# Optimization experiments

Hardware: AMD Instinct MI355X
Metric: run time of the kernel (lower is better)

The kernel has to match this reference:

```python
import jax, jax.numpy as jnp
import numpy as np

B, N, C = 16, 2048, 512
EPS = 1e-9        # numerical_stabilizer
BN_EPS = 1e-5     # flax BatchNorm default epsilon


def setup_inputs() -> dict:
    key = jax.random.key(0)
    ks = jax.random.split(key, 9)
    s = 1.0 / np.sqrt(C)

    def w(k):
        return jax.random.normal(k, (C, C), jnp.float32) * s

    return {
        "x": jax.random.normal(ks[0], (B, N, C), jnp.float32),
        "Wq": w(ks[1]), "bq": jnp.zeros((C,), jnp.float32),
        "Wk": w(ks[2]), "bk": jnp.zeros((C,), jnp.float32),
        "Wv": w(ks[3]), "bv": jnp.zeros((C,), jnp.float32),
        "Wo": w(ks[4]), "bo": jnp.zeros((C,), jnp.float32),
        "bn_scale": jnp.ones((C,), jnp.float32),
        "bn_bias": jnp.zeros((C,), jnp.float32),
        "bn_mean": jnp.zeros((C,), jnp.float32),
        "bn_var": jnp.ones((C,), jnp.float32),
    }


def reference(x, Wq, bq, Wk, bk, Wv, bv, Wo, bo,
              bn_scale, bn_bias, bn_mean, bn_var):
    # 1x1 'Conv' projections == pointwise linear layers
    q = x @ Wq + bq                                   # [B,N,C]
    k = x @ Wk + bk
    v = x @ Wv + bv

    # attention scores + row softmax
    att = jax.nn.softmax(jnp.einsum('bmc,bnc->bmn', q, k), axis=-1)  # [B,M,N]

    # post-softmax column renormalization: A / (eps + sum_M A),
    # then einsum '...MN,...NC->...NC' contracts M, so the effective
    # per-point scale is colsum / (eps + colsum).
    col = jnp.sum(att, axis=1)                        # [B,N]
    scale = col / (EPS + col)                         # [B,N]
    out = scale[..., None] * v                        # [B,N,C]

    # attention_type == 'naive': no offset
    y = out @ Wo + bo
    # BatchNorm with running stats (train=False)
    y = (y - bn_mean) * jax.lax.rsqrt(bn_var + BN_EPS) * bn_scale + bn_bias
    return jax.nn.relu(y) + x
```

## Files before the change

### kernel.cpp

```cpp
#include <hip/hip_runtime.h>
#include <math.h>

#define BB 16
#define NN 2048
#define CC 512
#define MM (BB * NN)
#define NSPLIT 4

typedef _Float16 half8 __attribute__((ext_vector_type(8)));
typedef _Float16 half4 __attribute__((ext_vector_type(4)));
typedef float floatx4 __attribute__((ext_vector_type(4)));

#define GLD16(gp, lp) __builtin_amdgcn_global_load_lds( \
    (const __attribute__((address_space(1))) void*)(gp), \
    (__attribute__((address_space(3))) void*)(lp), 16, 0, 0)

__device__ __forceinline__ int foff(int row16base, int fr, int g4) {
    return (row16base + fr) * 32 + ((g4 ^ ((fr >> 1) & 3)) << 3);
}

__global__ __launch_bounds__(256)
void calc_w2(const float* __restrict__ Wk, const float* __restrict__ bq,
             float* __restrict__ w2)
{
    const int i = blockIdx.x * 256 + threadIdx.x;
    if (i < 512) {
        float s = 0.0f;
        for (int j = 0; j < 512; ++j) s += Wk[i * 512 + j] * bq[j];
        w2[i] = s;
    }
}

__global__ __launch_bounds__(256)
void split_x_beta(const float* __restrict__ x, const float* __restrict__ w2,
                  _Float16* __restrict__ xh, _Float16* __restrict__ xl,
                  float* __restrict__ bet)
{
    __shared__ float part[4];
    const int t = threadIdx.x;
    const size_t i = (size_t)blockIdx.x * 1024 + (size_t)t * 4;
    const float4 v = *(const float4*)(x + i);
    half4 h, l;
    h[0] = (_Float16)v.x; l[0] = (_Float16)(v.x - (float)h[0]);
    h[1] = (_Float16)v.y; l[1] = (_Float16)(v.y - (float)h[1]);
    h[2] = (_Float16)v.z; l[2] = (_Float16)(v.z - (float)h[2]);
    h[3] = (_Float16)v.w; l[3] = (_Float16)(v.w - (float)h[3]);
    *(half4*)(xh + i) = h;
    *(half4*)(xl + i) = l;

    const float4 wv = *(const float4*)(w2 + ((t * 4) & 511));
    float s = v.x * wv.x + v.y * wv.y + v.z * wv.z + v.w * wv.w;
#pragma unroll
    for (int off = 1; off < 64; off <<= 1) s += __shfl_xor(s, off);
    const int w = t >> 6;
    if ((t & 63) == 0) part[w] = s;
    __syncthreads();
    const int m0 = blockIdx.x * 2;
    if (t == 0)   bet[m0]     = part[0] + part[1];
    if (t == 128) bet[m0 + 1] = part[2] + part[3];
}

__global__ __launch_bounds__(256)
void conv_wT(const float* __restrict__ W, _Float16* __restrict__ Wt)
{
    const int o = blockIdx.x * 256 + threadIdx.x;
    const int n = o >> 9, k = o & 511;
    Wt[o] = (_Float16)W[k * 512 + n];
}

__global__ __launch_bounds__(256)
void gemm_nt_split(const float* __restrict__ A, const float* __restrict__ Bm,
                   _Float16* __restrict__ outh, _Float16* __restrict__ outl)
{
    __shared__ float As[16][64];
    __shared__ float Bs[16][64];
    const int t = threadIdx.x, tc = t & 15, tr = t >> 4;
    const int j0 = blockIdx.x * 64, i0 = blockIdx.y * 64;
    const int lm = t >> 2, lk4 = (t & 3) << 2;
    float acc[4][4] = {};
    for (int kt = 0; kt < 512; kt += 16) {
        const float4 xa = *(const float4*)(A + (size_t)(j0 + lm) * 512 + kt + lk4);
        As[lk4 + 0][lm] = xa.x; As[lk4 + 1][lm] = xa.y;
        As[lk4 + 2][lm] = xa.z; As[lk4 + 3][lm] = xa.w;
        const float4 xb = *(const float4*)(Bm + (size_t)(i0 + lm) * 512 + kt + lk4);
        Bs[lk4 + 0][lm] = xb.x; Bs[lk4 + 1][lm] = xb.y;
        Bs[lk4 + 2][lm] = xb.z; Bs[lk4 + 3][lm] = xb.w;
        __syncthreads();
#pragma unroll
        for (int k = 0; k < 16; ++k) {
            float av[4], bv[4];
            *(float4*)av = *(const float4*)&As[k][tr * 4];
            *(float4*)bv = *(const float4*)&Bs[k][tc * 4];
#pragma unroll
            for (int i = 0; i < 4; ++i)
#pragma unroll
                for (int j = 0; j < 4; ++j)
                    acc[i][j] = fmaf(av[i], bv[j], acc[i][j]);
        }
        __syncthreads();
    }
#pragma unroll
    for (int i = 0; i < 4; ++i) {
        const int row = j0 + tr * 4 + i;
#pragma unroll
        for (int j = 0; j < 4; ++j) {
            const int col = i0 + tc * 4 + j;
            const float y = acc[i][j];
            const _Float16 h = (_Float16)y;
            outh[row * 512 + col] = h;
            outl[row * 512 + col] = (_Float16)(y - (float)h);
        }
    }
}

__global__ __launch_bounds__(256)
void gemm16_split(const _Float16* __restrict__ Ah, const _Float16* __restrict__ Al,
                  const _Float16* __restrict__ Bh, const _Float16* __restrict__ Bl,
                  _Float16* __restrict__ oh, _Float16* __restrict__ ol)
{
    __shared__ __align__(16) _Float16 sAh[128 * 32], sBh[128 * 32];
    __shared__ __align__(16) _Float16 sAl[128 * 32], sBl[128 * 32];

    const int t = threadIdx.x, lane = t & 63, w = t >> 6;
    const int m0 = blockIdx.x * 128, n0 = blockIdx.y * 128;
    const int lr4 = lane >> 2;
    const int sw8 = (((lane & 3) ^ ((lr4 >> 1) & 3)) << 3);
    const int fr = lane & 15, g4 = lane >> 4;
    const int wr = (w >> 1) * 64, wc = (w & 1) * 64;

    floatx4 acc[4][4];
#pragma unroll
    for (int i = 0; i < 4; ++i)
#pragma unroll
        for (int j = 0; j < 4; ++j) acc[i][j] = (floatx4){0.f, 0.f, 0.f, 0.f};

    for (int kt = 0; kt < CC; kt += 32) {
#pragma unroll
        for (int c = 0; c < 2; ++c) {
            const int r = w * 32 + c * 16;
            const size_t goA = (size_t)(m0 + r + lr4) * CC + kt + sw8;
            const size_t goB = (size_t)(n0 + r + lr4) * CC + kt + sw8;
            GLD16(Ah + goA, sAh + r * 32);
            GLD16(Bh + goB, sBh + r * 32);
            GLD16(Al + goA, sAl + r * 32);
            GLD16(Bl + goB, sBl + r * 32);
        }
        __syncthreads();

        half8 fa[4], fb[4], fal[4], fbl[4];
#pragma unroll
        for (int rt = 0; rt < 4; ++rt) {
            fa[rt]  = *(const half8*)&sAh[foff(wr + rt * 16, fr, g4)];
            fal[rt] = *(const half8*)&sAl[foff(wr + rt * 16, fr, g4)];
        }
#pragma unroll
        for (int ct = 0; ct < 4; ++ct) {
            fb[ct]  = *(const half8*)&sBh[foff(wc + ct * 16, fr, g4)];
            fbl[ct] = *(const half8*)&sBl[foff(wc + ct * 16, fr, g4)];
        }
#pragma unroll
        for (int rt = 0; rt < 4; ++rt)
#pragma unroll
            for (int ct = 0; ct < 4; ++ct) {
                acc[rt][ct] = __builtin_amdgcn_mfma_f32_16x16x32_f16(
                    fa[rt], fb[ct], acc[rt][ct], 0, 0, 0);
                acc[rt][ct] = __builtin_amdgcn_mfma_f32_16x16x32_f16(
                    fa[rt], fbl[ct], acc[rt][ct], 0, 0, 0);
                acc[rt][ct] = __builtin_amdgcn_mfma_f32_16x16x32_f16(
                    fal[rt], fb[ct], acc[rt][ct], 0, 0, 0);
            }
        __syncthreads();
    }

#pragma unroll
    for (int rt = 0; rt < 4; ++rt)
#pragma unroll
        for (int ct = 0; ct < 4; ++ct) {
            const int col = n0 + wc + ct * 16 + fr;
#pragma unroll
            for (int reg = 0; reg < 4; ++reg) {
                const int row = m0 + wr + rt * 16 + g4 * 4 + reg;
                const float y = acc[rt][ct][reg];
                const _Float16 h = (_Float16)y;
                oh[(size_t)row * CC + col] = h;
                ol[(size_t)row * CC + col] = (_Float16)(y - (float)h);
            }
        }
}

template<int MODE>
__global__ __launch_bounds__(256, 2)
void gemm16n(const _Float16* __restrict__ Ah, const _Float16* __restrict__ Bh,
             const float* __restrict__ bias, const float* __restrict__ colsc,
             const float* __restrict__ bn_scale, const float* __restrict__ bn_bias,
             const float* __restrict__ bn_mean, const float* __restrict__ bn_var,
             const float* __restrict__ xres,
             _Float16* __restrict__ oh, float* __restrict__ outf)
{
    __shared__ __align__(16) _Float16 sA0[128 * 32], sA1[128 * 32], sA2[128 * 32];
    __shared__ __align__(16) _Float16 sB0[256 * 32], sB1[256 * 32], sB2[256 * 32];

    const int t = threadIdx.x, lane = t & 63, w = t >> 6;
    const int m0 = blockIdx.x * 128, n0 = blockIdx.y * 256;
    const int lr4 = lane >> 2;
    const int sw8 = (((lane & 3) ^ ((lr4 >> 1) & 3)) << 3);
    const int fr = lane & 15, g4 = lane >> 4;
    const int wr = (w >> 1) * 64, wc = (w & 1) * 128;

    floatx4 acc[4][8];
#pragma unroll
    for (int i = 0; i < 4; ++i)
#pragma unroll
        for (int j = 0; j < 8; ++j) acc[i][j] = (floatx4){0.f, 0.f, 0.f, 0.f};

    auto stage = [&](_Float16* Sa, _Float16* Sb, int gt) {
        const int kt = gt * 32;
#pragma unroll
        for (int c = 0; c < 2; ++c) {
            const int r = w * 32 + c * 16;
            GLD16(Ah + (size_t)(m0 + r + lr4) * CC + kt + sw8, Sa + r * 32);
        }
#pragma unroll
        for (int c = 0; c < 4; ++c) {
            const int r = w * 64 + c * 16;
            GLD16(Bh + (size_t)(n0 + r + lr4) * CC + kt + sw8, Sb + r * 32);
        }
    };

    auto tile = [&](const _Float16* Ra, const _Float16* Rb,
                    _Float16* Sa, _Float16* Sb, int gt, int mode) {
        if (mode == 0) stage(Sa, Sb, gt + 2);
        half8 fa[4];
#pragma unroll
        for (int rt = 0; rt < 4; ++rt)
            fa[rt] = *(const half8*)&Ra[foff(wr + rt * 16, fr, g4)];
#pragma unroll
        for (int hh = 0; hh < 2; ++hh) {
            half8 fb[4];
#pragma unroll
            for (int c4 = 0; c4 < 4; ++c4)
                fb[c4] = *(const half8*)&Rb[foff(wc + (hh * 4 + c4) * 16, fr, g4)];
            __builtin_amdgcn_s_setprio(1);
#pragma unroll
            for (int rt = 0; rt < 4; ++rt)
#pragma unroll
                for (int c4 = 0; c4 < 4; ++c4)
                    acc[rt][hh * 4 + c4] = __builtin_amdgcn_mfma_f32_16x16x32_f16(
                        fa[rt], fb[c4], acc[rt][hh * 4 + c4], 0, 0, 0);
            __builtin_amdgcn_s_setprio(0);
        }
        if (mode == 0)      asm volatile("s_waitcnt vmcnt(6)" ::: "memory");
        else if (mode == 1) asm volatile("s_waitcnt vmcnt(0)" ::: "memory");
        __builtin_amdgcn_s_barrier();
        asm volatile("" ::: "memory");
    };

    stage(sA0, sB0, 0);
    stage(sA1, sB1, 1);
    asm volatile("s_waitcnt vmcnt(6)" ::: "memory");
    __builtin_amdgcn_s_barrier();
    asm volatile("" ::: "memory");

#pragma unroll 1
    for (int u = 0; u < 4; ++u) {
        const int gt = u * 3;
        tile(sA0, sB0, sA2, sB2, gt,     0);
        tile(sA1, sB1, sA0, sB0, gt + 1, 0);
        tile(sA2, sB2, sA1, sB1, gt + 2, 0);
    }
    tile(sA0, sB0, sA2, sB2, 12, 0);
    tile(sA1, sB1, sA0, sB0, 13, 0);
    tile(sA2, sB2, nullptr, nullptr, 14, 1);
    tile(sA0, sB0, nullptr, nullptr, 15, 2);

#pragma unroll
    for (int rt = 0; rt < 4; ++rt)
#pragma unroll
        for (int ct = 0; ct < 8; ++ct) {
            const int col = n0 + wc + ct * 16 + fr;
#pragma unroll
            for (int reg = 0; reg < 4; ++reg) {
                const int row = m0 + wr + rt * 16 + g4 * 4 + reg;
                float y = acc[rt][ct][reg];
                if constexpr (MODE == 1) {
                    y = (y + bias[col]) * colsc[row];
                    oh[(size_t)row * CC + col] = (_Float16)y;
                } else {
                    y += bias[col];
                    y = (y - bn_mean[col]) * rsqrtf(bn_var[col] + 1e-5f)
                            * bn_scale[col] + bn_bias[col];
                    y = fmaxf(y, 0.0f) + xres[(size_t)row * CC + col];
                    outf[(size_t)row * CC + col] = y;
                }
            }
        }
}

__device__ __forceinline__ void attn_decode3(int& xt, int& b, int& sp) {
    const int h = blockIdx.x + (blockIdx.y << 4) + (blockIdx.z << 8);
    xt = (h >> 3) & 15;
    const int g = ((h >> 7) << 3) | (h & 7);
    b = g & 15;
    sp = g >> 4;
}
__device__ __forceinline__ void attn_decode_col(int& xt, int& b, int& sp) {
    const int h = blockIdx.x + (blockIdx.y << 3) + (blockIdx.z << 7);
    xt = (h >> 3) & 7;
    const int g = ((h >> 6) << 3) | (h & 7);
    b = g & 15;
    sp = g >> 4;
}

__global__ __launch_bounds__(256, 2)
void attn_rowstats(const _Float16* __restrict__ ah_, const _Float16* __restrict__ al_,
                   const _Float16* __restrict__ xh_,
                   const float* __restrict__ bet,
                   float* __restrict__ pm, float* __restrict__ pl)
{
    __shared__ __align__(16) _Float16 A0[128 * 32], A1[128 * 32], A2[128 * 32];
    __shared__ __align__(16) _Float16 X0[256 * 32], X1[256 * 32], X2[256 * 32];
    __shared__ float wm[4][64], wl[4][64];

    int xt, b, sp;
    attn_decode3(xt, b, sp);
    const int m0 = xt * 128;
    const int t = threadIdx.x, lane = t & 63, w = t >> 6;
    const int lr4 = lane >> 2;
    const int sw8 = (((lane & 3) ^ ((lr4 >> 1) & 3)) << 3);
    const int fr = lane & 15, g4 = lane >> 4;
    const int wr = (w >> 1) * 64, wc = (w & 1) * 128;
    const size_t bbase = (size_t)b * NN;

    float betA[8], betB[8];
#pragma unroll
    for (int ct = 0; ct < 8; ++ct) {
        betA[ct] = bet[bbase + sp * 512 +   0 + wc + ct * 16 + fr];
        betB[ct] = bet[bbase + sp * 512 + 256 + wc + ct * 16 + fr];
    }

    float m_st[4][4], l_st[4][4];
#pragma unroll
    for (int i = 0; i < 4; ++i)
#pragma unroll
        for (int j = 0; j < 4; ++j) { m_st[i][j] = -3.0e38f; l_st[i][j] = 0.0f; }

    floatx4 acc[4][8];
#pragma unroll
    for (int i = 0; i < 4; ++i)
#pragma unroll
        for (int j = 0; j < 8; ++j) acc[i][j] = (floatx4){0.f, 0.f, 0.f, 0.f};

    auto stage = [&](_Float16* Sa, _Float16* Sx, int gt) {
        const int nn0 = sp * 512 + (gt >> 4) * 256;
        const int nkt = (gt & 15) * 32;
#pragma unroll
        for (int c = 0; c < 2; ++c) {
            const int r = w * 32 + c * 16;
            GLD16(ah_ + (bbase + m0 + r + lr4) * CC + nkt + sw8, Sa + r * 32);
        }
#pragma unroll
        for (int c = 0; c < 4; ++c) {
            const int r = w * 64 + c * 16;
            GLD16(xh_ + (bbase + nn0 + r + lr4) * CC + nkt + sw8, Sx + r * 32);
        }
    };

    auto tile = [&](const _Float16* Ra, const _Float16* Rx,
                    _Float16* Sa, _Float16* Sx, int gt, int mode) {
        const int kt = (gt & 15) * 32;
        half8 fal[4];
#pragma unroll
        for (int rt = 0; rt < 4; ++rt)
            fal[rt] = *(const half8*)(al_ + (bbase + m0 + wr + rt * 16 + fr) * CC
                                      + kt + g4 * 8);
        if (mode == 0) stage(Sa, Sx, gt + 2);
        half8 fa[4];
#pragma unroll
        for (int rt = 0; rt < 4; ++rt)
            fa[rt] = *(const half8*)&Ra[foff(wr + rt * 16, fr, g4)];
#pragma unroll
        for (int hh = 0; hh < 2; ++hh) {
            half8 fb[4];
#pragma unroll
            for (int c4 = 0; c4 < 4; ++c4)
                fb[c4] = *(const half8*)&Rx[foff(wc + (hh * 4 + c4) * 16, fr, g4)];
            __builtin_amdgcn_s_setprio(1);
#pragma unroll
            for (int rt = 0; rt < 4; ++rt)
#pragma unroll
                for (int c4 = 0; c4 < 4; ++c4) {
                    acc[rt][hh * 4 + c4] = __builtin_amdgcn_mfma_f32_16x16x32_f16(
                        fa[rt], fb[c4], acc[rt][hh * 4 + c4], 0, 0, 0);
                    acc[rt][hh * 4 + c4] = __builtin_amdgcn_mfma_f32_16x16x32_f16(
                        fal[rt], fb[c4], acc[rt][hh * 4 + c4], 0, 0, 0);
                }
            __builtin_amdgcn_s_setprio(0);
        }
        if ((gt & 15) == 15) {
            const bool c1 = (gt >> 4) != 0;
#pragma unroll
            for (int rt = 0; rt < 4; ++rt)
#pragma unroll
                for (int reg = 0; reg < 4; ++reg) {
                    float v[8];
#pragma unroll
                    for (int ct = 0; ct < 8; ++ct)
                        v[ct] = acc[rt][ct][reg] + (c1 ? betB[ct] : betA[ct]);
                    float mx = v[0];
#pragma unroll
                    for (int ct = 1; ct < 8; ++ct) mx = fmaxf(mx, v[ct]);
                    const float mo = m_st[rt][reg];
                    const float mn = fmaxf(mo, mx);
                    float s = 0.0f;
#pragma unroll
                    for (int ct = 0; ct < 8; ++ct) s += __expf(v[ct] - mn);
                    l_st[rt][reg] = l_st[rt][reg] * __expf(mo - mn) + s;
                    m_st[rt][reg] = mn;
                }
#pragma unroll
            for (int i = 0; i < 4; ++i)
#pragma unroll
                for (int j = 0; j < 8; ++j) acc[i][j] = (floatx4){0.f, 0.f, 0.f, 0.f};
        }
        if (mode == 0)      asm volatile("s_waitcnt vmcnt(6)" ::: "memory");
        else if (mode == 1) asm volatile("s_waitcnt vmcnt(0)" ::: "memory");
        __builtin_amdgcn_s_barrier();
        asm volatile("" ::: "memory");
    };

    stage(A0, X0, 0);
    stage(A1, X1, 1);
    asm volatile("s_waitcnt vmcnt(6)" ::: "memory");
    __builtin_amdgcn_s_barrier();
    asm volatile("" ::: "memory");

#pragma unroll 1
    for (int u = 0; u < 10; ++u) {
        const int gt = u * 3;
        tile(A0, X0, A2, X2, gt,     0);
        tile(A1, X1, A0, X0, gt + 1, 0);
        tile(A2, X2, A1, X1, gt + 2, 0);
    }
    tile(A0, X0, nullptr, nullptr, 30, 1);
    tile(A1, X1, nullptr, nullptr, 31, 2);

#pragma unroll
    for (int rt = 0; rt < 4; ++rt)
#pragma unroll
        for (int reg = 0; reg < 4; ++reg) {
            float m = m_st[rt][reg], l = l_st[rt][reg];
#pragma unroll
            for (int off = 1; off < 16; off <<= 1) {
                const float mo = __shfl_xor(m, off);
                const float lo = __shfl_xor(l, off);
                const float mn = fmaxf(m, mo);
                l = l * __expf(m - mn) + lo * __expf(mo - mn);
                m = mn;
            }
            if (fr == 0) {
                wm[w][rt * 16 + g4 * 4 + reg] = m;
                wl[w][rt * 16 + g4 * 4 + reg] = l;
            }
        }
    __syncthreads();
    if (t < 128) {
        const int r = t & 63;
        const int wa = (t < 64) ? 0 : 2, wb = wa + 1;
        const float ma = wm[wa][r], mb = wm[wb][r];
        const float M = fmaxf(ma, mb);
        const float L = wl[wa][r] * __expf(ma - M) + wl[wb][r] * __expf(mb - M);
        pm[(size_t)sp * MM + bbase + m0 + t] = M;
        pl[(size_t)sp * MM + bbase + m0 + t] = L;
    }
}

__global__ __launch_bounds__(256)
void rho_merge(const float* __restrict__ pm, const float* __restrict__ pl,
               float* __restrict__ rho)
{
    const size_t i = (size_t)blockIdx.x * 256 + threadIdx.x;
    float M = pm[i];
#pragma unroll
    for (int s = 1; s < NSPLIT; ++s) M = fmaxf(M, pm[s * (size_t)MM + i]);
    float L = 0.0f;
#pragma unroll
    for (int s = 0; s < NSPLIT; ++s)
        L += pl[s * (size_t)MM + i] * __expf(pm[s * (size_t)MM + i] - M);
    rho[i] = M + __logf(L);
}

__global__ __launch_bounds__(256, 2)
void attn_colsum(const _Float16* __restrict__ ah_, const _Float16* __restrict__ al_,
                 const _Float16* __restrict__ xh_,
                 const float* __restrict__ bet, const float* __restrict__ rho,
                 float* __restrict__ pc)
{
    __shared__ __align__(16) _Float16 A0[128 * 32], A1[128 * 32], A2[128 * 32];
    __shared__ __align__(16) _Float16 X0[256 * 32], X1[256 * 32], X2[256 * 32];
    __shared__ float cred[4][128];

    int xt, b, sp;
    attn_decode_col(xt, b, sp);
    const int n0 = xt * 256;
    const int t = threadIdx.x, lane = t & 63, w = t >> 6;
    const int lr4 = lane >> 2;
    const int sw8 = (((lane & 3) ^ ((lr4 >> 1) & 3)) << 3);
    const int fr = lane & 15, g4 = lane >> 4;
    const int wr = (w >> 1) * 64, wc = (w & 1) * 128;
    const size_t bbase = (size_t)b * NN;

    float bet_r[8];
#pragma unroll
    for (int ct = 0; ct < 8; ++ct)
        bet_r[ct] = bet[bbase + n0 + wc + ct * 16 + fr];

    float csum[8] = {0.f, 0.f, 0.f, 0.f, 0.f, 0.f, 0.f, 0.f};
    floatx4 rr[4];
    floatx4 acc[4][8];
#pragma unroll
    for (int i = 0; i < 4; ++i)
#pragma unroll
        for (int j = 0; j < 8; ++j) acc[i][j] = (floatx4){0.f, 0.f, 0.f, 0.f};

    auto stage = [&](_Float16* Sa, _Float16* Sx, int gt) {
        const int nm0 = sp * 512 + (gt >> 4) * 128;
        const int nkt = (gt & 15) * 32;
#pragma unroll
        for (int c = 0; c < 2; ++c) {
            const int r = w * 32 + c * 16;
            GLD16(ah_ + (bbase + nm0 + r + lr4) * CC + nkt + sw8, Sa + r * 32);
        }
#pragma unroll
        for (int c = 0; c < 4; ++c) {
            const int r = w * 64 + c * 16;
            GLD16(xh_ + (bbase + n0 + r + lr4) * CC + nkt + sw8, Sx + r * 32);
        }
    };

    auto tile = [&](const _Float16* Ra, const _Float16* Rx,
                    _Float16* Sa, _Float16* Sx, int gt, int mode) {
        const int kt = (gt & 15) * 32;
        const int m0c = sp * 512 + (gt >> 4) * 128;
        if ((gt & 15) == 0) {
#pragma unroll
            for (int rt = 0; rt < 4; ++rt)
                rr[rt] = *(const floatx4*)&rho[bbase + m0c + wr + rt * 16 + g4 * 4];
        }
        half8 fal[4];
#pragma unroll
        for (int rt = 0; rt < 4; ++rt)
            fal[rt] = *(const half8*)(al_ + (bbase + m0c + wr + rt * 16 + fr) * CC
                                      + kt + g4 * 8);
        if (mode == 0) stage(Sa, Sx, gt + 2);
        half8 fa[4];
#pragma unroll
        for (int rt = 0; rt < 4; ++rt)
            fa[rt] = *(const half8*)&Ra[foff(wr + rt * 16, fr, g4)];
#pragma unroll
        for (int hh = 0; hh < 2; ++hh) {
            half8 fb[4];
#pragma unroll
            for (int c4 = 0; c4 < 4; ++c4)
                fb[c4] = *(const half8*)&Rx[foff(wc + (hh * 4 + c4) * 16, fr, g4)];
            __builtin_amdgcn_s_setprio(1);
#pragma unroll
            for (int rt = 0; rt < 4; ++rt)
#pragma unroll
                for (int c4 = 0; c4 < 4; ++c4) {
                    acc[rt][hh * 4 + c4] = __builtin_amdgcn_mfma_f32_16x16x32_f16(
                        fa[rt], fb[c4], acc[rt][hh * 4 + c4], 0, 0, 0);
                    acc[rt][hh * 4 + c4] = __builtin_amdgcn_mfma_f32_16x16x32_f16(
                        fal[rt], fb[c4], acc[rt][hh * 4 + c4], 0, 0, 0);
                }
            __builtin_amdgcn_s_setprio(0);
        }
        if ((gt & 15) == 15) {
#pragma unroll
            for (int rt = 0; rt < 4; ++rt)
#pragma unroll
                for (int reg = 0; reg < 4; ++reg) {
                    const float r = rr[rt][reg];
#pragma unroll
                    for (int ct = 0; ct < 8; ++ct)
                        csum[ct] += __expf(acc[rt][ct][reg] + bet_r[ct] - r);
                }
#pragma unroll
            for (int i = 0; i < 4; ++i)
#pragma unroll
                for (int j = 0; j < 8; ++j) acc[i][j] = (floatx4){0.f, 0.f, 0.f, 0.f};
        }
        if (mode == 0)      asm volatile("s_waitcnt vmcnt(6)" ::: "memory");
        else if (mode == 1) asm volatile("s_waitcnt vmcnt(0)" ::: "memory");
        __builtin_amdgcn_s_barrier();
        asm volatile("" ::: "memory");
    };

    stage(A0, X0, 0);
    stage(A1, X1, 1);
    asm volatile("s_waitcnt vmcnt(6)" ::: "memory");
    __builtin_amdgcn_s_barrier();
    asm volatile("" ::: "memory");

#pragma unroll 1
    for (int u = 0; u < 20; ++u) {
        const int gt = u * 3;
        tile(A0, X0, A2, X2, gt,     0);
        tile(A1, X1, A0, X0, gt + 1, 0);
        tile(A2, X2, A1, X1, gt + 2, 0);
    }
    tile(A0, X0, A2, X2, 60, 0);
    tile(A1, X1, A0, X0, 61, 0);
    tile(A2, X2, nullptr, nullptr, 62, 1);
    tile(A0, X0, nullptr, nullptr, 63, 2);

#pragma unroll
    for (int ct = 0; ct < 8; ++ct) {
        csum[ct] += __shfl_xor(csum[ct], 16);
        csum[ct] += __shfl_xor(csum[ct], 32);
    }
    if (lane < 16)
#pragma unroll
        for (int ct = 0; ct < 8; ++ct) cred[w][ct * 16 + lane] = csum[ct];
    __syncthreads();
    if (t < 256) {
        const int c = t & 127;
        const float s = (t < 128) ? (cred[0][c] + cred[2][c])
                                  : (cred[1][c] + cred[3][c]);
        pc[(size_t)sp * MM + bbase + n0 + t] = s;
    }
}

__global__ __launch_bounds__(256)
void colsc_merge(const float* __restrict__ pc, float* __restrict__ colsc)
{
    const size_t i = (size_t)blockIdx.x * 256 + threadIdx.x;
    float c = 0.0f;
#pragma unroll
    for (int s = 0; s < NSPLIT; ++s) c += pc[s * (size_t)MM + i];
    colsc[i] = c / (1e-9f + c);
}

extern "C" void kernel_launch(void* const* d_in, const int* in_sizes, int n_in,
                              void* d_out, int out_size, void* d_ws, size_t ws_size,
                              hipStream_t stream)
{
    const float* x        = (const float*)d_in[0];
    const float* Wq       = (const float*)d_in[1];
    const float* bq       = (const float*)d_in[2];
    const float* Wk       = (const float*)d_in[3];
    const float* bk       = (const float*)d_in[4];   (void)bk;
    const float* Wv       = (const float*)d_in[5];
    const float* bv       = (const float*)d_in[6];
    const float* Wo       = (const float*)d_in[7];
    const float* bo       = (const float*)d_in[8];
    const float* bn_scale = (const float*)d_in[9];
    const float* bn_bias  = (const float*)d_in[10];
    const float* bn_mean  = (const float*)d_in[11];
    const float* bn_var   = (const float*)d_in[12];
    float* out = (float*)d_out;

    const size_t MMC = (size_t)MM * CC;
    _Float16* xh = (_Float16*)d_ws;
    _Float16* xl = xh + MMC;
    _Float16* ah = xl + MMC;
    _Float16* al = ah + MMC;
    _Float16* th  = al;
    _Float16* Wvt = ah;
    _Float16* Wot = ah + 512 * 512;

    char* ob = (char*)d_out;
    _Float16* Pth = (_Float16*)(ob);
    _Float16* Ptl = (_Float16*)(ob + (1u << 19));
    float* w2     = (float*)(ob + (2u << 19));
    float* bet    = (float*)(ob + (2u << 19) + 8192);
    float* rho    = (float*)(ob + 1318912);
    float* colsc  = (float*)(ob + 1449984);
    float* pm     = (float*)(ob + 1581056);
    float* pl     = (float*)(ob + 2105344);
    float* pc     = (float*)(ob + 2629632);

    const dim3 blk(256);
    const dim3 ga(MM / 128, CC / 128);
    const dim3 gn(MM / 128, CC / 256);
    const dim3 grow(NN / 128, BB, NSPLIT);
    const dim3 gcol(NN / 256, BB, NSPLIT);

    calc_w2<<<2, blk, 0, stream>>>(Wk, bq, w2);
    split_x_beta<<<MMC / 1024, blk, 0, stream>>>(x, w2, xh, xl, bet);
    gemm_nt_split<<<dim3(8, 8), blk, 0, stream>>>(Wk, Wq, Pth, Ptl);

    gemm16_split<<<ga, blk, 0, stream>>>(xh, xl, Pth, Ptl, ah, al);

    attn_rowstats<<<grow, blk, 0, stream>>>(ah, al, xh, bet, pm, pl);
    rho_merge<<<MM / 256, blk, 0, stream>>>(pm, pl, rho);
    attn_colsum<<<gcol, blk, 0, stream>>>(ah, al, xh, bet, rho, pc);
    colsc_merge<<<MM / 256, blk, 0, stream>>>(pc, colsc);

    conv_wT<<<1024, blk, 0, stream>>>(Wv, Wvt);
    gemm16n<1><<<gn, blk, 0, stream>>>(xh, Wvt, bv, colsc,
        nullptr, nullptr, nullptr, nullptr, nullptr, th, nullptr);

    conv_wT<<<1024, blk, 0, stream>>>(Wo, Wot);
    gemm16n<2><<<gn, blk, 0, stream>>>(th, Wot, bo, nullptr,
        bn_scale, bn_bias, bn_mean, bn_var, x, nullptr, out);
}
```

Before: 589.1 us.

## Triple-buffer split-fp16 GEMM with async LDS prefetch and direct Bl global loads

Replaces the single-buffered load/sync/compute loop in gemm16_split with a three-stage LDS ring, prefetching tile k+2 while computing tile k. A single barrier per tile is kept, with hand-placed vmcnt waits. The B low-part operand is now read straight from global memory into registers instead of staged through LDS, which reduces LDS traffic. It also raises MFMA issue priority with s_setprio and sets a two-blocks-per-CU occupancy hint. The risks are that the larger LDS footprint (72KB) and the manual waitcnt counting may limit occupancy or introduce ordering mistakes.

```diff
diff --git a/kernel.cpp b/kernel.cpp
--- a/kernel.cpp
+++ b/kernel.cpp
@@ -113,13 +113,14 @@
     }
 }
 
-__global__ __launch_bounds__(256)
+__global__ __launch_bounds__(256, 2)
 void gemm16_split(const _Float16* __restrict__ Ah, const _Float16* __restrict__ Al,
                   const _Float16* __restrict__ Bh, const _Float16* __restrict__ Bl,
                   _Float16* __restrict__ oh, _Float16* __restrict__ ol)
 {
-    __shared__ __align__(16) _Float16 sAh[128 * 32], sBh[128 * 32];
-    __shared__ __align__(16) _Float16 sAl[128 * 32], sBl[128 * 32];
+    __shared__ __align__(16) _Float16 sA0[128 * 32], sA1[128 * 32], sA2[128 * 32];
+    __shared__ __align__(16) _Float16 sL0[128 * 32], sL1[128 * 32], sL2[128 * 32];
+    __shared__ __align__(16) _Float16 sB0[128 * 32], sB1[128 * 32], sB2[128 * 32];
 
     const int t = threadIdx.x, lane = t & 63, w = t >> 6;
     const int m0 = blockIdx.x * 128, n0 = blockIdx.y * 128;
@@ -134,30 +135,38 @@
 #pragma unroll
         for (int j = 0; j < 4; ++j) acc[i][j] = (floatx4){0.f, 0.f, 0.f, 0.f};
 
-    for (int kt = 0; kt < CC; kt += 32) {
+    auto stage = [&](_Float16* Sa, _Float16* Sl, _Float16* Sb, int gt) {
+        const int kt = gt * 32;
 #pragma unroll
         for (int c = 0; c < 2; ++c) {
             const int r = w * 32 + c * 16;
             const size_t goA = (size_t)(m0 + r + lr4) * CC + kt + sw8;
             const size_t goB = (size_t)(n0 + r + lr4) * CC + kt + sw8;
-            GLD16(Ah + goA, sAh + r * 32);
-            GLD16(Bh + goB, sBh + r * 32);
-            GLD16(Al + goA, sAl + r * 32);
-            GLD16(Bl + goB, sBl + r * 32);
-        }
-        __syncthreads();
-
-        half8 fa[4], fb[4], fal[4], fbl[4];
+            GLD16(Ah + goA, Sa + r * 32);
+            GLD16(Al + goA, Sl + r * 32);
+            GLD16(Bh + goB, Sb + r * 32);
+        }
+    };
+
+    auto tile = [&](const _Float16* Ra, const _Float16* Rl, const _Float16* Rb,
+                    _Float16* Sa, _Float16* Sl, _Float16* Sb, int gt, int mode) {
+        const int kt = gt * 32;
+        half8 fbl[4];
+#pragma unroll
+        for (int ct = 0; ct < 4; ++ct)
+            fbl[ct] = *(const half8*)(Bl + (size_t)(n0 + wc + ct * 16 + fr) * CC
+                                      + kt + g4 * 8);
+        if (mode == 0) stage(Sa, Sl, Sb, gt + 2);
+        half8 fa[4], fal[4], fb[4];
 #pragma unroll
         for (int rt = 0; rt < 4; ++rt) {
-            fa[rt]  = *(const half8*)&sAh[foff(wr + rt * 16, fr, g4)];
-            fal[rt] = *(const half8*)&sAl[foff(wr + rt * 16, fr, g4)];
-        }
-#pragma unroll
-        for (int ct = 0; ct < 4; ++ct) {
-            fb[ct]  = *(const half8*)&sBh[foff(wc + ct * 16, fr, g4)];
-            fbl[ct] = *(const half8*)&sBl[foff(wc + ct * 16, fr, g4)];
-        }
+            fa[rt]  = *(const half8*)&Ra[foff(wr + rt * 16, fr, g4)];
+            fal[rt] = *(const half8*)&Rl[foff(wr + rt * 16, fr, g4)];
+        }
+#pragma unroll
+        for (int ct = 0; ct < 4; ++ct)
+            fb[ct] = *(const half8*)&Rb[foff(wc + ct * 16, fr, g4)];
+        __builtin_amdgcn_s_setprio(1);
 #pragma unroll
         for (int rt = 0; rt < 4; ++rt)
 #pragma unroll
@@ -169,8 +178,30 @@
                 acc[rt][ct] = __builtin_amdgcn_mfma_f32_16x16x32_f16(
                     fal[rt], fb[ct], acc[rt][ct], 0, 0, 0);
             }
-        __syncthreads();
-    }
+        __builtin_amdgcn_s_setprio(0);
+        if (mode == 0)      asm volatile("s_waitcnt vmcnt(6)" ::: "memory");
+        else if (mode == 1) asm volatile("s_waitcnt vmcnt(0)" ::: "memory");
+        __builtin_amdgcn_s_barrier();
+        asm volatile("" ::: "memory");
+    };
+
+    stage(sA0, sL0, sB0, 0);
+    stage(sA1, sL1, sB1, 1);
+    asm volatile("s_waitcnt vmcnt(6)" ::: "memory");
+    __builtin_amdgcn_s_barrier();
+    asm volatile("" ::: "memory");
+
+#pragma unroll 1
+    for (int u = 0; u < 4; ++u) {
+        const int gt = u * 3;
+        tile(sA0, sL0, sB0, sA2, sL2, sB2, gt,     0);
+        tile(sA1, sL1, sB1, sA0, sL0, sB0, gt + 1, 0);
+        tile(sA2, sL2, sB2, sA1, sL1, sB1, gt + 2, 0);
+    }
+    tile(sA0, sL0, sB0, sA2, sL2, sB2, 12, 0);
+    tile(sA1, sL1, sB1, sA0, sL0, sB0, 13, 0);
+    tile(sA2, sL2, sB2, nullptr, nullptr, nullptr, 14, 1);
+    tile(sA0, sL0, sB0, nullptr, nullptr, nullptr, 15, 2);
 
 #pragma unroll
     for (int rt = 0; rt < 4; ++rt)
```

Measured after the change: 620.0 us. 1.05x slower.
